# Optimization experiments

Measured on AMD Instinct MI355X. Metric: run time of the kernel, lower is better.

Reference implementation:

```python
import jax, jax.numpy as jnp
import numpy as np

S = 2_000_000   # sequence length (tokens/residues)
P = 1_000_000   # number of 'positive' (pu) indices
E = 20          # number of experts / alphabet size


def setup_inputs() -> dict:
    key = jax.random.key(0)
    k1, k2, k3, k4, k5 = jax.random.split(key, 5)
    # x[0, :, :20] acts as per-token one-hot over the 20-letter alphabet;
    # argmax of uniform noise gives a valid routing index per token.
    x = jax.random.uniform(k1, (1, S, E), dtype=jnp.float32)
    h = jax.random.normal(k2, (S, 2), dtype=jnp.float32)        # 'output1' from inner model
    W = jax.random.normal(k3, (E, 2, 2), dtype=jnp.float32) * 0.5  # per-expert Linear weight [out,in]
    b = jax.random.normal(k4, (E, 2), dtype=jnp.float32) * 0.1     # per-expert Linear bias
    # unique, sorted positive indices (torch.index_select semantics)
    pu_index = jnp.sort(jax.random.permutation(k5, S)[:P]).astype(jnp.int32)
    return {"x": x, "h": h, "W": W, "b": b, "pu_index": pu_index}


def reference(x, h, W, b, pu_index):
    # recognize_res: per-token expert index from one-hot channels 0:20 of x[0]
    res_index = jnp.argmax(x[0, :, :E], axis=-1)                 # [S] int
    # verblizer_function: per-token expert Linear(2,2) + Softmax, fused as
    # gather expert params -> batched matmul -> softmax
    Wt = W[res_index]                                            # [S, 2, 2]
    bt = b[res_index]                                            # [S, 2]
    y = jnp.einsum('si,soi->so', h, Wt) + bt                     # torch Linear: h @ W.T + b
    y = jax.nn.softmax(y, axis=-1)                               # output1 after verblizer
    # pu_train: rows at pu_index first (in pu order), remaining rows after
    n_tok = h.shape[0]
    mask = jnp.zeros((n_tok,), dtype=bool).at[pu_index].set(True)
    non = jnp.nonzero(~mask, size=n_tok - pu_index.shape[0])[0]  # preserves original order
    perm = jnp.concatenate([pu_index.astype(non.dtype), non])
    y2 = y[perm]                                                 # output2
    return (y, y2)
```

## Files before the change

kernel.cpp:

```cpp
#include <hip/hip_runtime.h>
#include <math.h>

#define TPB  256
#define TILE 512
#define GRAN 64

__global__ __launch_bounds__(TPB) void boundary_kernel(
    const int* __restrict__ pu, int P, int NB, int* __restrict__ boundary)
{
    int i = blockIdx.x * TPB + threadIdx.x;
    if (i >= P) return;
    int cur = pu[i];
    int lo  = (i == 0) ? 0 : (pu[i - 1] / GRAN) + 1;
    int hi  = cur / GRAN;
    for (int bb = lo; bb <= hi; ++bb) boundary[bb] = i;
    if (i == P - 1)
        for (int bb = hi + 1; bb <= NB; ++bb) boundary[bb] = P;
}

__global__ __launch_bounds__(TPB) void verblizer_fused_kernel(
    const float4* __restrict__ x4,
    const float2* __restrict__ h2,
    const float*  __restrict__ W,
    const float*  __restrict__ b,
    const int*    __restrict__ pu,
    const int*    __restrict__ boundary,
    float2*       __restrict__ y,
    float2*       __restrict__ y2,
    int S, int P)
{
    const int t    = threadIdx.x;
    const int lane = t & 63;
    const int w    = t >> 6;
    const int B0   = min((int)blockIdx.x * TILE, S - TILE);

    const int base = B0 + 128 * w;
    const int s0   = base + lane;
    const int s1   = base + 64 + lane;

    const int wi  = __builtin_amdgcn_readfirstlane(base >> 6);
    const int rA0 = boundary[wi];
    const int rA1 = boundary[wi + 1];
    const int rB1 = boundary[wi + 2];

    const int pA = pu[min(rA0 + lane, P - 1)];
    const int pB = pu[min(rA1 + lane, P - 1)];

    float4 xa[5], xbv[5];
    const float4* xp0 = x4 + (size_t)s0 * 5;
    const float4* xp1 = x4 + (size_t)s1 * 5;
#pragma unroll
    for (int c = 0; c < 5; ++c) { xa[c] = xp0[c]; xbv[c] = xp1[c]; }
    const float2 h0 = h2[s0];
    const float2 h1 = h2[s1];

    const int nA = rA1 - rA0;
    const int nB = rB1 - rA1;
    unsigned long long mA = (lane < nA) ? (1ull << ((unsigned)(pA - base) & 63)) : 0ull;
    unsigned long long mB = (lane < nB) ? (1ull << ((unsigned)(pB - base - 64) & 63)) : 0ull;
#pragma unroll
    for (int d = 1; d < 64; d <<= 1) {
        mA |= __shfl_xor(mA, d, 64);
        mB |= __shfl_xor(mB, d, 64);
    }
    const unsigned long long lt = (1ull << lane) - 1ull;
    const int  rankA = rA0 + __popcll(mA & lt);
    const int  rankB = rA1 + __popcll(mB & lt);
    const bool fA    = (mA >> lane) & 1;
    const bool fB    = (mB >> lane) & 1;

#pragma unroll
    for (int half = 0; half < 2; ++half) {
        const float4* xv  = half ? xbv : xa;
        const float2  hv  = half ? h1 : h0;
        const int     s   = half ? s1 : s0;
        const bool    f   = half ? fB : fA;
        const int     rnk = half ? rankB : rankA;

        float best = -INFINITY; int bi = 0;
#pragma unroll
        for (int c = 0; c < 5; ++c) {
            float4 v = xv[c];
            if (v.x > best) { best = v.x; bi = 4 * c + 0; }
            if (v.y > best) { best = v.y; bi = 4 * c + 1; }
            if (v.z > best) { best = v.z; bi = 4 * c + 2; }
            if (v.w > best) { best = v.w; bi = 4 * c + 3; }
        }

        const float4 wv = *(const float4*)(W + bi * 4);
        const float2 bv = *(const float2*)(b + bi * 2);
        float y0 = fmaf(hv.x, wv.x, fmaf(hv.y, wv.y, bv.x));
        float y1 = fmaf(hv.x, wv.z, fmaf(hv.y, wv.w, bv.y));
        float mx = fmaxf(y0, y1);
        float e0 = __expf(y0 - mx);
        float e1 = __expf(y1 - mx);
        float inv = 1.0f / (e0 + e1);
        float2 yo = make_float2(e0 * inv, e1 * inv);

        y[s] = yo;
        const int dst = f ? rnk : (P + s - rnk);
        y2[dst] = yo;
    }
}

extern "C" void kernel_launch(void* const* d_in, const int* in_sizes, int n_in,
                              void* d_out, int out_size, void* d_ws, size_t ws_size,
                              hipStream_t stream) {
    const float* x  = (const float*)d_in[0];
    const float* h  = (const float*)d_in[1];
    const float* W  = (const float*)d_in[2];
    const float* b  = (const float*)d_in[3];
    const int*   pu = (const int*)d_in[4];

    const int S  = in_sizes[1] / 2;
    const int P  = in_sizes[4];
    const int NB = S / GRAN;

    int* boundary = (int*)d_ws;

    float2* y  = (float2*)d_out;
    float2* y2 = (float2*)d_out + S;

    boundary_kernel<<<(P + TPB - 1) / TPB, TPB, 0, stream>>>(pu, P, NB, boundary);

    const int grid = (S + TILE - 1) / TILE;
    verblizer_fused_kernel<<<grid, TPB, 0, stream>>>(
        (const float4*)x, (const float2*)h, W, b, pu, boundary, y, y2, S, P);
}
```

Before: 254.9 us.

## Coalesce x loads across wave and reduce argmax partials through LDS

Each wave now loads the 64 tokens' x rows as contiguous float4s striped across lanes (coalesced), instead of each lane reading its own 5 float4s at a stride of 80 bytes. Each lane computes a partial argmax over its float4 and writes it to shared memory, then each lane reduces the 5 partials for its own token. Tokens per thread drop from two to one, so the grid doubles. This trades LDS traffic and more blocks for better global-load coalescing of the dominant 160 MB x read.

```diff
diff --git a/kernel.cpp b/kernel.cpp
--- a/kernel.cpp
+++ b/kernel.cpp
@@ -2,7 +2,6 @@
 #include <math.h>
 
 #define TPB  256
-#define TILE 512
 #define GRAN 64
 
 __global__ __launch_bounds__(TPB) void boundary_kernel(
@@ -29,78 +28,70 @@
     float2*       __restrict__ y2,
     int S, int P)
 {
+    __shared__ uint2 scratch[(TPB / 64) * 320];
+
     const int t    = threadIdx.x;
     const int lane = t & 63;
     const int w    = t >> 6;
-    const int B0   = min((int)blockIdx.x * TILE, S - TILE);
+    const int B0   = min((int)blockIdx.x * TPB, S - TPB);
 
-    const int base = B0 + 128 * w;
-    const int s0   = base + lane;
-    const int s1   = base + 64 + lane;
+    const int base = B0 + 64 * w;
+    const int s    = base + lane;
 
-    const int wi  = __builtin_amdgcn_readfirstlane(base >> 6);
-    const int rA0 = boundary[wi];
-    const int rA1 = boundary[wi + 1];
-    const int rB1 = boundary[wi + 2];
+    const int wi = __builtin_amdgcn_readfirstlane(base >> 6);
+    const int r0 = boundary[wi];
+    const int r1 = boundary[wi + 1];
 
-    const int pA = pu[min(rA0 + lane, P - 1)];
-    const int pB = pu[min(rA1 + lane, P - 1)];
+    float4 xv[5];
+    const float4* xp = x4 + (size_t)base * 5;
+#pragma unroll
+    for (int j = 0; j < 5; ++j) xv[j] = xp[64 * j + lane];
 
-    float4 xa[5], xbv[5];
-    const float4* xp0 = x4 + (size_t)s0 * 5;
-    const float4* xp1 = x4 + (size_t)s1 * 5;
+    const float2 hv = h2[s];
+    const int    pv = pu[min(r0 + lane, P - 1)];
+
+    const int nmark = r1 - r0;
+    unsigned long long m =
+        (lane < nmark) ? (1ull << ((unsigned)(pv - base) & 63)) : 0ull;
 #pragma unroll
-    for (int c = 0; c < 5; ++c) { xa[c] = xp0[c]; xbv[c] = xp1[c]; }
-    const float2 h0 = h2[s0];
-    const float2 h1 = h2[s1];
+    for (int d = 1; d < 64; d <<= 1) m |= __shfl_xor(m, d, 64);
+    const int  rank = r0 + __popcll(m & ((1ull << lane) - 1ull));
+    const bool f    = (m >> lane) & 1;
 
-    const int nA = rA1 - rA0;
-    const int nB = rB1 - rA1;
-    unsigned long long mA = (lane < nA) ? (1ull << ((unsigned)(pA - base) & 63)) : 0ull;
-    unsigned long long mB = (lane < nB) ? (1ull << ((unsigned)(pB - base - 64) & 63)) : 0ull;
+    uint2* sw = scratch + w * 320;
 #pragma unroll
-    for (int d = 1; d < 64; d <<= 1) {
-        mA |= __shfl_xor(mA, d, 64);
-        mB |= __shfl_xor(mB, d, 64);
+    for (int j = 0; j < 5; ++j) {
+        float4 v = xv[j];
+        float best = v.x; int bi = 0;
+        if (v.y > best) { best = v.y; bi = 1; }
+        if (v.z > best) { best = v.z; bi = 2; }
+        if (v.w > best) { best = v.w; bi = 3; }
+        const int flat = 64 * j + lane;
+        const int c    = flat % 5;
+        sw[flat] = make_uint2(__float_as_uint(best), (unsigned)(4 * c + bi));
     }
-    const unsigned long long lt = (1ull << lane) - 1ull;
-    const int  rankA = rA0 + __popcll(mA & lt);
-    const int  rankB = rA1 + __popcll(mB & lt);
-    const bool fA    = (mA >> lane) & 1;
-    const bool fB    = (mB >> lane) & 1;
 
+    float best = -INFINITY; int bi = 0;
 #pragma unroll
-    for (int half = 0; half < 2; ++half) {
-        const float4* xv  = half ? xbv : xa;
-        const float2  hv  = half ? h1 : h0;
-        const int     s   = half ? s1 : s0;
-        const bool    f   = half ? fB : fA;
-        const int     rnk = half ? rankB : rankA;
+    for (int c = 0; c < 5; ++c) {
+        uint2 p = sw[5 * lane + c];
+        float v = __uint_as_float(p.x);
+        if (v > best) { best = v; bi = (int)p.y; }
+    }
 
-        float best = -INFINITY; int bi = 0;
-#pragma unroll
-        for (int c = 0; c < 5; ++c) {
-            float4 v = xv[c];
-            if (v.x > best) { best = v.x; bi = 4 * c + 0; }
-            if (v.y > best) { best = v.y; bi = 4 * c + 1; }
-            if (v.z > best) { best = v.z; bi = 4 * c + 2; }
-            if (v.w > best) { best = v.w; bi = 4 * c + 3; }
-        }
+    const float4 wv = *(const float4*)(W + bi * 4);
+    const float2 bv = *(const float2*)(b + bi * 2);
+    float y0 = fmaf(hv.x, wv.x, fmaf(hv.y, wv.y, bv.x));
+    float y1 = fmaf(hv.x, wv.z, fmaf(hv.y, wv.w, bv.y));
+    float mx = fmaxf(y0, y1);
+    float e0 = __expf(y0 - mx);
+    float e1 = __expf(y1 - mx);
+    float inv = 1.0f / (e0 + e1);
+    float2 yo = make_float2(e0 * inv, e1 * inv);
 
-        const float4 wv = *(const float4*)(W + bi * 4);
-        const float2 bv = *(const float2*)(b + bi * 2);
-        float y0 = fmaf(hv.x, wv.x, fmaf(hv.y, wv.y, bv.x));
-        float y1 = fmaf(hv.x, wv.z, fmaf(hv.y, wv.w, bv.y));
-        float mx = fmaxf(y0, y1);
-        float e0 = __expf(y0 - mx);
-        float e1 = __expf(y1 - mx);
-        float inv = 1.0f / (e0 + e1);
-        float2 yo = make_float2(e0 * inv, e1 * inv);
-
-        y[s] = yo;
-        const int dst = f ? rnk : (P + s - rnk);
-        y2[dst] = yo;
-    }
+    y[s] = yo;
+    const int dst = f ? rank : (P + s - rank);
+    y2[dst] = yo;
 }
 
 extern "C" void kernel_launch(void* const* d_in, const int* in_sizes, int n_in,
@@ -123,7 +114,7 @@
 
     boundary_kernel<<<(P + TPB - 1) / TPB, TPB, 0, stream>>>(pu, P, NB, boundary);
 
-    const int grid = (S + TILE - 1) / TILE;
+    const int grid = (S + TPB - 1) / TPB;
     verblizer_fused_kernel<<<grid, TPB, 0, stream>>>(
         (const float4*)x, (const float2*)h, W, b, pu, boundary, y, y2, S, P);
 }
```

Result: no change. 251.7 us (-1.2%).
